# Kernel tuning notes

Measured on AMD Instinct MI355X. Metric: run time of the kernel, lower is better.

Reference implementation:

```python
import jax, jax.numpy as jnp
import numpy as np

B, T, L = 256, 2048, 48  # batch, seq_len, nb_labels


def setup_inputs() -> dict:
    key = jax.random.key(0)
    k1, k2, k3 = jax.random.split(key, 3)
    emissions = jax.random.normal(k1, (B, T, L), dtype=jnp.float32)
    tags = jax.random.randint(k2, (B, T), 0, L, dtype=jnp.int32)
    # matches nn.init.uniform_(transitions, -0.1, 0.1)
    transitions = jax.random.uniform(k3, (L, L), dtype=jnp.float32, minval=-0.1, maxval=0.1)
    return {"emissions": emissions, "tags": tags, "transitions": transitions}


def _gold_scores(emissions, tags, transitions):
    # emission score at every gold tag: [B, T] -> sum over T
    e = jnp.take_along_axis(emissions, tags[..., None], axis=2)[..., 0].sum(axis=1)
    # transition scores between consecutive gold tags
    t = transitions[tags[:, :-1], tags[:, 1:]].sum(axis=1)
    start = transitions[0, tags[:, 0]]      # row 0 acts as start scores
    end = transitions[tags[:, -1], -1]      # last column acts as end scores
    return e + t + start + end              # [B]


def _log_partition(emissions, transitions):
    # forward algorithm: alpha_t[b, j] = logsumexp_i(alpha_{t-1}[b, i] + T[i, j]) + em[b, t, j]
    alpha0 = transitions[0][None, :] + emissions[:, 0]          # [B, L]
    em_rest = jnp.moveaxis(emissions[:, 1:], 1, 0)              # [T-1, B, L]

    def step(alpha, em_t):
        alpha = jax.nn.logsumexp(alpha[:, :, None] + transitions[None, :, :], axis=1) + em_t
        return alpha, None

    alpha, _ = jax.lax.scan(step, alpha0, em_rest)
    return jax.nn.logsumexp(alpha + transitions[:, -1][None, :], axis=1)  # [B]


def reference(emissions, tags, transitions):
    """neg_log_likelihood of LinearChainCRF: -sum(scores - log_partition)."""
    scores = _gold_scores(emissions, tags, transitions)
    partition = _log_partition(emissions, transitions)
    return -jnp.sum(scores - partition)
```

## Files before the change

### kernel.cpp

```cpp
#include <hip/hip_runtime.h>

#define B 256
#define T 2048
#define L 48
#define G 16
#define SEG 128
#define KNORM 4.371f
#define TOTALF (B * T * L)

typedef short v4s __attribute__((ext_vector_type(4)));
typedef float v4f __attribute__((ext_vector_type(4)));
typedef int   v2i __attribute__((ext_vector_type(2)));

#define WAVE_SYNC() asm volatile("s_waitcnt lgkmcnt(0)" ::: "memory")

#if __has_builtin(__builtin_amdgcn_mfma_f32_16x16x16bf16_1k)
#define MFMA16(a, b, c) __builtin_amdgcn_mfma_f32_16x16x16bf16_1k((a), (b), (c), 0, 0, 0)
#else
__device__ __forceinline__ v4f mfma16_asm(v4s a, v4s b, v4f c) {
    asm volatile("v_mfma_f32_16x16x16_bf16 %0, %1, %2, %0\n\ts_nop 7\n\ts_nop 7"
                 : "+v"(c) : "v"(a), "v"(b));
    return c;
}
#define MFMA16(a, b, c) mfma16_asm((a), (b), (c))
#endif

__device__ __forceinline__ unsigned pk_bf16(float lo, float hi) {
#if __has_builtin(__builtin_amdgcn_cvt_pk_bf16_f32)
    auto r = __builtin_amdgcn_cvt_pk_bf16_f32(lo, hi);
    unsigned u;
    __builtin_memcpy(&u, &r, 4);
    return u;
#else
    unsigned uh = __float_as_uint(hi) + 0x8000u;
    unsigned ul = __float_as_uint(lo) + 0x8000u;
    return __builtin_amdgcn_perm(uh, ul, 0x07060302u);
#endif
}

__device__ __forceinline__ v4s scale_pack(v4f cf, v4f g) {
    float a0 = cf.x * g.x, a1 = cf.y * g.y;
    float a2 = cf.z * g.z, a3 = cf.w * g.w;
    v2i d;
    d.x = (int)pk_bf16(a0, a1);
    d.y = (int)pk_bf16(a2, a3);
    return __builtin_bit_cast(v4s, d);
}

__global__ __launch_bounds__(64, 4) void crf_scan(
    const float* __restrict__ em, const int* __restrict__ tags,
    const float* __restrict__ trans, float* __restrict__ out,
    float* __restrict__ ws)
{
    const int b = blockIdx.x >> 4;
    const int s = blockIdx.x & 15;
    const int j = threadIdx.x;
    const int q = j >> 4;
    const int c = j & 15;

    __shared__ __align__(16) float smem[2 * 384];

    const size_t bem = (size_t)b * T * L;
    const int t0 = 1 + SEG * s;
    const int t1 = (t0 + SEG < T) ? (t0 + SEG) : T;

    v4s Af[3][3];
    #pragma unroll
    for (int rt = 0; rt < 3; ++rt)
        #pragma unroll
        for (int kt = 0; kt < 3; ++kt) {
            v4f e;
            #pragma unroll
            for (int ee = 0; ee < 4; ++ee)
                e[ee] = __expf(trans[(16 * kt + 4 * q + ee) * L + 16 * rt + c]);
            Af[rt][kt] = scale_pack(e, v4f{1.f, 1.f, 1.f, 1.f});
        }

    v4s Bq[3][3];
    #pragma unroll
    for (int kt = 0; kt < 3; ++kt)
        #pragma unroll
        for (int ct = 0; ct < 3; ++ct) {
            v2i d;
            int k0 = 16 * kt + 4 * q, col = 16 * ct + c;
            d.x = (k0 + 0 == col ? 0x3F80 : 0) | (k0 + 1 == col ? 0x3F800000 : 0);
            d.y = (k0 + 2 == col ? 0x3F80 : 0) | (k0 + 3 == col ? 0x3F800000 : 0);
            Bq[kt][ct] = __builtin_bit_cast(v4s, d);
        }

    auto do_step = [&](const float* rowp) {
        v4f gv[3];
        #pragma unroll
        for (int rt = 0; rt < 3; ++rt)
            gv[rt] = *(const v4f*)(rowp + 16 * rt + 4 * q);
        v4s Bn[3][3];
        #pragma unroll
        for (int rt = 0; rt < 3; ++rt)
            #pragma unroll
            for (int ct = 0; ct < 3; ++ct) {
                v4f acc = {0.f, 0.f, 0.f, 0.f};
                acc = MFMA16(Af[rt][0], Bq[0][ct], acc);
                acc = MFMA16(Af[rt][1], Bq[1][ct], acc);
                acc = MFMA16(Af[rt][2], Bq[2][ct], acc);
                Bn[rt][ct] = scale_pack(acc, gv[rt]);
            }
        #pragma unroll
        for (int rt = 0; rt < 3; ++rt)
            #pragma unroll
            for (int ct = 0; ct < 3; ++ct)
                Bq[rt][ct] = Bn[rt][ct];
    };

    {
        size_t gf = bem + (size_t)t0 * L;
        #pragma unroll
        for (int ch = 0; ch < 6; ++ch)
            smem[64 * ch + j] = __expf(em[gf + 64 * ch + j] - KNORM);
        WAVE_SYNC();
    }

    for (int bk = 0; bk < 16; ++bk) {
        const float* cur = smem + (bk & 1) * 384;
        float* nxt = smem + ((bk & 1) ^ 1) * 384;

        size_t gf = bem + (size_t)(t0 + 8 * (bk + 1)) * L;
        if (gf > (size_t)TOTALF - 384) gf = (size_t)TOTALF - 384;
        float stg[6];
        #pragma unroll
        for (int ch = 0; ch < 6; ++ch) stg[ch] = em[gf + 64 * ch + j];

        #pragma unroll
        for (int k = 0; k < 8; ++k)
            if (t0 + 8 * bk + k < t1)
                do_step(cur + 48 * k);

        #pragma unroll
        for (int ch = 0; ch < 6; ++ch)
            nxt[64 * ch + j] = __expf(stg[ch] - KNORM);
        WAVE_SYNC();
    }

    unsigned short* qs = (unsigned short*)ws + (size_t)(b * G + s) * 2304;
    #pragma unroll
    for (int kt = 0; kt < 3; ++kt)
        #pragma unroll
        for (int ct = 0; ct < 3; ++ct) {
            v2i d = __builtin_bit_cast(v2i, Bq[kt][ct]);
            int r0 = 16 * kt + 4 * q, col = 16 * ct + c;
            qs[(r0 + 0) * 48 + col] = (unsigned short)((unsigned)d.x & 0xffffu);
            qs[(r0 + 1) * 48 + col] = (unsigned short)((unsigned)d.x >> 16);
            qs[(r0 + 2) * 48 + col] = (unsigned short)((unsigned)d.y & 0xffffu);
            qs[(r0 + 3) * 48 + col] = (unsigned short)((unsigned)d.y >> 16);
        }

    const int* tg = tags + (size_t)b * T;
    float gp = 0.f;
    #pragma unroll
    for (int r = 0; r < 2; ++r) {
        int t = SEG * s + 64 * r + j;
        int tag = tg[t];
        gp += em[bem + (size_t)t * L + tag];
        if (t < T - 1)  gp += trans[tag * L + tg[t + 1]];
        if (t == 0)     gp += trans[tag];
        if (t == T - 1) gp += trans[tag * L + (L - 1)];
    }
    #pragma unroll
    for (int off = 32; off; off >>= 1) gp += __shfl_xor(gp, off);
    if (j == 0) atomicAdd(out, -gp);
}

__global__ __launch_bounds__(64) void crf_combine(
    const float* __restrict__ em, const float* __restrict__ trans,
    const float* __restrict__ ws, float* __restrict__ out)
{
    const int b = blockIdx.x, l = threadIdx.x;
    const int lc = (l < L) ? l : (L - 1);

    __shared__ float us[64];

    const unsigned short* qb = (const unsigned short*)ws + (size_t)b * G * 2304;

    float u = (l < L) ? __expf(trans[l] + em[(size_t)b * T * L + l]) : 0.f;
    float logtot = 2047.0f * KNORM;

    uint4 pre[6];
    {
        const uint4* p = (const uint4*)(qb + lc * 48);
        #pragma unroll
        for (int ii = 0; ii < 6; ++ii) pre[ii] = p[ii];
    }

    for (int s = 0; s < G; ++s) {
        us[l] = u;
        uint4 cur[6];
        #pragma unroll
        for (int ii = 0; ii < 6; ++ii) cur[ii] = pre[ii];
        if (s + 1 < G) {
            const uint4* p = (const uint4*)(qb + (size_t)(s + 1) * 2304 + lc * 48);
            #pragma unroll
            for (int ii = 0; ii < 6; ++ii) pre[ii] = p[ii];
        }
        WAVE_SYNC();

        float acc = 0.f;
        #pragma unroll
        for (int ii = 0; ii < 6; ++ii) {
            unsigned w0 = cur[ii].x, w1 = cur[ii].y, w2 = cur[ii].z, w3 = cur[ii].w;
            int jj = ii * 8;
            acc = fmaf(__uint_as_float(w0 << 16),          us[jj + 0], acc);
            acc = fmaf(__uint_as_float(w0 & 0xffff0000u),  us[jj + 1], acc);
            acc = fmaf(__uint_as_float(w1 << 16),          us[jj + 2], acc);
            acc = fmaf(__uint_as_float(w1 & 0xffff0000u),  us[jj + 3], acc);
            acc = fmaf(__uint_as_float(w2 << 16),          us[jj + 4], acc);
            acc = fmaf(__uint_as_float(w2 & 0xffff0000u),  us[jj + 5], acc);
            acc = fmaf(__uint_as_float(w3 << 16),          us[jj + 6], acc);
            acc = fmaf(__uint_as_float(w3 & 0xffff0000u),  us[jj + 7], acc);
        }
        WAVE_SYNC();

        float r = __int_as_float(
            __builtin_amdgcn_readlane(__float_as_int(acc), 0));
        logtot += __logf(r);
        u = (l < L) ? acc * __builtin_amdgcn_rcpf(r) : 0.f;
    }

    float v = (l < L) ? u * __expf(trans[lc * L + (L - 1)]) : 0.f;
    #pragma unroll
    for (int off = 32; off; off >>= 1) v += __shfl_xor(v, off);
    if (l == 0) atomicAdd(out, logtot + __logf(v));
}

extern "C" void kernel_launch(void* const* d_in, const int* in_sizes, int n_in,
                              void* d_out, int out_size, void* d_ws, size_t ws_size,
                              hipStream_t stream) {
    const float* em    = (const float*)d_in[0];
    const int*   tags  = (const int*)  d_in[1];
    const float* trans = (const float*)d_in[2];
    float* out = (float*)d_out;
    float* ws  = (float*)d_ws;

    (void)hipMemsetAsync(out, 0, sizeof(float), stream);
    crf_scan   <<<B * G, 64, 0, stream>>>(em, tags, trans, out, ws);
    crf_combine<<<B,     64, 0, stream>>>(em, trans, ws, out);
}
```

Before: 282.4 us.

## Split segment matrix product across three waves, one per column tile

The scan block grows from one wave to three. Each wave owns one 16-column tile of the 48x48 segment transfer matrix, so the dependent chain per time step drops from 27 MFMAs to 9 per wave and register pressure falls. Emission staging is spread over 192 threads, and the gold-score partial sums are reduced through shared memory before one atomic per block. The cost is a block-wide barrier every 8 steps in place of the wave-local wait, and more total waves competing for each CU.

```diff
diff --git a/kernel.cpp b/kernel.cpp
--- a/kernel.cpp
+++ b/kernel.cpp
@@ -47,16 +47,18 @@
     return __builtin_bit_cast(v4s, d);
 }
 
-__global__ __launch_bounds__(64, 4) void crf_scan(
+__global__ __launch_bounds__(192, 6) void crf_scan(
     const float* __restrict__ em, const int* __restrict__ tags,
     const float* __restrict__ trans, float* __restrict__ out,
     float* __restrict__ ws)
 {
-    const int b = blockIdx.x >> 4;
-    const int s = blockIdx.x & 15;
-    const int j = threadIdx.x;
-    const int q = j >> 4;
-    const int c = j & 15;
+    const int b   = blockIdx.x >> 4;
+    const int s   = blockIdx.x & 15;
+    const int tid = threadIdx.x;
+    const int ct  = tid >> 6;
+    const int ln  = tid & 63;
+    const int q   = ln >> 4;
+    const int c   = ln & 15;
 
     __shared__ __align__(16) float smem[2 * 384];
 
@@ -76,47 +78,40 @@
             Af[rt][kt] = scale_pack(e, v4f{1.f, 1.f, 1.f, 1.f});
         }
 
-    v4s Bq[3][3];
-    #pragma unroll
-    for (int kt = 0; kt < 3; ++kt)
-        #pragma unroll
-        for (int ct = 0; ct < 3; ++ct) {
-            v2i d;
-            int k0 = 16 * kt + 4 * q, col = 16 * ct + c;
-            d.x = (k0 + 0 == col ? 0x3F80 : 0) | (k0 + 1 == col ? 0x3F800000 : 0);
-            d.y = (k0 + 2 == col ? 0x3F80 : 0) | (k0 + 3 == col ? 0x3F800000 : 0);
-            Bq[kt][ct] = __builtin_bit_cast(v4s, d);
-        }
+    v4s Bq[3];
+    #pragma unroll
+    for (int kt = 0; kt < 3; ++kt) {
+        v2i d;
+        int k0 = 16 * kt + 4 * q, col = 16 * ct + c;
+        d.x = (k0 + 0 == col ? 0x3F80 : 0) | (k0 + 1 == col ? 0x3F800000 : 0);
+        d.y = (k0 + 2 == col ? 0x3F80 : 0) | (k0 + 3 == col ? 0x3F800000 : 0);
+        Bq[kt] = __builtin_bit_cast(v4s, d);
+    }
 
     auto do_step = [&](const float* rowp) {
         v4f gv[3];
         #pragma unroll
         for (int rt = 0; rt < 3; ++rt)
             gv[rt] = *(const v4f*)(rowp + 16 * rt + 4 * q);
-        v4s Bn[3][3];
+        v4f Cf[3];
+        #pragma unroll
+        for (int rt = 0; rt < 3; ++rt) {
+            v4f acc = {0.f, 0.f, 0.f, 0.f};
+            acc = MFMA16(Af[rt][0], Bq[0], acc);
+            acc = MFMA16(Af[rt][1], Bq[1], acc);
+            acc = MFMA16(Af[rt][2], Bq[2], acc);
+            Cf[rt] = acc;
+        }
         #pragma unroll
         for (int rt = 0; rt < 3; ++rt)
-            #pragma unroll
-            for (int ct = 0; ct < 3; ++ct) {
-                v4f acc = {0.f, 0.f, 0.f, 0.f};
-                acc = MFMA16(Af[rt][0], Bq[0][ct], acc);
-                acc = MFMA16(Af[rt][1], Bq[1][ct], acc);
-                acc = MFMA16(Af[rt][2], Bq[2][ct], acc);
-                Bn[rt][ct] = scale_pack(acc, gv[rt]);
-            }
-        #pragma unroll
-        for (int rt = 0; rt < 3; ++rt)
-            #pragma unroll
-            for (int ct = 0; ct < 3; ++ct)
-                Bq[rt][ct] = Bn[rt][ct];
+            Bq[rt] = scale_pack(Cf[rt], gv[rt]);
     };
 
     {
         size_t gf = bem + (size_t)t0 * L;
-        #pragma unroll
-        for (int ch = 0; ch < 6; ++ch)
-            smem[64 * ch + j] = __expf(em[gf + 64 * ch + j] - KNORM);
-        WAVE_SYNC();
+        smem[tid]       = __expf(em[gf + tid]       - KNORM);
+        smem[tid + 192] = __expf(em[gf + tid + 192] - KNORM);
+        __syncthreads();
     }
 
     for (int bk = 0; bk < 16; ++bk) {
@@ -125,39 +120,34 @@
 
         size_t gf = bem + (size_t)(t0 + 8 * (bk + 1)) * L;
         if (gf > (size_t)TOTALF - 384) gf = (size_t)TOTALF - 384;
-        float stg[6];
-        #pragma unroll
-        for (int ch = 0; ch < 6; ++ch) stg[ch] = em[gf + 64 * ch + j];
+        float stg0 = em[gf + tid];
+        float stg1 = em[gf + tid + 192];
 
         #pragma unroll
         for (int k = 0; k < 8; ++k)
             if (t0 + 8 * bk + k < t1)
                 do_step(cur + 48 * k);
 
-        #pragma unroll
-        for (int ch = 0; ch < 6; ++ch)
-            nxt[64 * ch + j] = __expf(stg[ch] - KNORM);
-        WAVE_SYNC();
+        nxt[tid]       = __expf(stg0 - KNORM);
+        nxt[tid + 192] = __expf(stg1 - KNORM);
+        __syncthreads();
     }
 
     unsigned short* qs = (unsigned short*)ws + (size_t)(b * G + s) * 2304;
     #pragma unroll
-    for (int kt = 0; kt < 3; ++kt)
-        #pragma unroll
-        for (int ct = 0; ct < 3; ++ct) {
-            v2i d = __builtin_bit_cast(v2i, Bq[kt][ct]);
-            int r0 = 16 * kt + 4 * q, col = 16 * ct + c;
-            qs[(r0 + 0) * 48 + col] = (unsigned short)((unsigned)d.x & 0xffffu);
-            qs[(r0 + 1) * 48 + col] = (unsigned short)((unsigned)d.x >> 16);
-            qs[(r0 + 2) * 48 + col] = (unsigned short)((unsigned)d.y & 0xffffu);
-            qs[(r0 + 3) * 48 + col] = (unsigned short)((unsigned)d.y >> 16);
-        }
+    for (int kt = 0; kt < 3; ++kt) {
+        v2i d = __builtin_bit_cast(v2i, Bq[kt]);
+        int r0 = 16 * kt + 4 * q, col = 16 * ct + c;
+        qs[(r0 + 0) * 48 + col] = (unsigned short)((unsigned)d.x & 0xffffu);
+        qs[(r0 + 1) * 48 + col] = (unsigned short)((unsigned)d.x >> 16);
+        qs[(r0 + 2) * 48 + col] = (unsigned short)((unsigned)d.y & 0xffffu);
+        qs[(r0 + 3) * 48 + col] = (unsigned short)((unsigned)d.y >> 16);
+    }
 
     const int* tg = tags + (size_t)b * T;
     float gp = 0.f;
-    #pragma unroll
-    for (int r = 0; r < 2; ++r) {
-        int t = SEG * s + 64 * r + j;
+    if (tid < 128) {
+        int t = SEG * s + tid;
         int tag = tg[t];
         gp += em[bem + (size_t)t * L + tag];
         if (t < T - 1)  gp += trans[tag * L + tg[t + 1]];
@@ -166,7 +156,10 @@
     }
     #pragma unroll
     for (int off = 32; off; off >>= 1) gp += __shfl_xor(gp, off);
-    if (j == 0) atomicAdd(out, -gp);
+    __shared__ float red[3];
+    if (ln == 0) red[ct] = gp;
+    __syncthreads();
+    if (tid == 0) atomicAdd(out, -(red[0] + red[1] + red[2]));
 }
 
 __global__ __launch_bounds__(64) void crf_combine(
@@ -240,6 +233,6 @@
     float* ws  = (float*)d_ws;
 
     (void)hipMemsetAsync(out, 0, sizeof(float), stream);
-    crf_scan   <<<B * G, 64, 0, stream>>>(em, tags, trans, out, ws);
-    crf_combine<<<B,     64, 0, stream>>>(em, trans, ws, out);
-}
+    crf_scan   <<<B * G, 192, 0, stream>>>(em, tags, trans, out, ws);
+    crf_combine<<<B,      64, 0, stream>>>(em, trans, ws, out);
+}
```

After: 267.6 us. -5.2%, faster.
